# Kernel tuning notes

Hardware: AMD Instinct MI355X
Metric: run time of the kernel (lower is better)

Reference implementation:

```python
import jax, jax.numpy as jnp
import numpy as np

B, C, H, W = 4, 64, 600, 600  # batch, out channels, spatial (H, W divisible by 5)

def setup_inputs() -> dict:
    key = jax.random.key(0)
    k1, k2, k3 = jax.random.split(key, 3)
    x = jax.random.normal(k1, (B, 1, H, W), dtype=jnp.float32)
    # Conv2d(1, channels, kernel_size=3) params; the torch module always uses conv_list[0]
    fan_in = 1 * 3 * 3
    bound = 1.0 / np.sqrt(fan_in)
    weight = jax.random.uniform(k2, (C, 1, 3, 3), dtype=jnp.float32, minval=-bound, maxval=bound)
    bias = jax.random.uniform(k3, (C,), dtype=jnp.float32, minval=-bound, maxval=bound)
    return {"x": x, "weight": weight, "bias": bias}

def reference(x, weight, bias):
    # The 25-phase roll + unfold(stride=5) + fold(stride=3) + conv(stride=3) + strided
    # scatter is exactly a circularly-padded 3x3 stride-1 cross-correlation:
    #   out[b,c,y,xx] = sum_{r,s} weight[c,0,r,s] * x[b,0,(y-1+r)%H,(xx-1+s)%W] + bias[c]
    xp = jnp.pad(x, ((0, 0), (0, 0), (1, 1), (1, 1)), mode="wrap")  # circular pad by 1
    out = jax.lax.conv_general_dilated(
        xp, weight,
        window_strides=(1, 1), padding="VALID",
        dimension_numbers=("NCHW", "OIHW", "NCHW"),
    )
    return out + bias[None, :, None, None]
```

## Files before the change

### kernel.cpp

```cpp
#include <hip/hip_runtime.h>


typedef float v4f __attribute__((ext_vector_type(4)));

#define Bn 4
#define Cn 64
#define Hn 600
#define Wn 600
#define Gn (Wn / 4)
#define TOTAL (Bn * Hn * Gn)

__global__ __launch_bounds__(256) void conv3x3_circ_kernel(
    const float* __restrict__ x,
    const float* __restrict__ w,
    const float* __restrict__ bias,
    float* __restrict__ out)
{
    __shared__ float lw[Cn * 12];
    const int tid = threadIdx.x;
    for (int idx = tid; idx < Cn * 12; idx += 256) {
        const int c = idx / 12;
        const int k = idx - c * 12;
        float v = 0.0f;
        if (k < 9)       v = w[c * 9 + k];
        else if (k == 9) v = bias[c];
        lw[idx] = v;
    }
    __syncthreads();

    const int i = blockIdx.x * 256 + tid;
    if (i >= TOTAL) return;

    const int g  = i % Gn;
    const int t  = i / Gn;
    const int y  = t % Hn;
    const int b  = t / Hn;
    const int x0 = g * 4;

    const int ym = (y == 0)        ? (Hn - 1) : (y - 1);
    const int yp = (y == Hn - 1)   ? 0        : (y + 1);
    const int xm = (x0 == 0)       ? (Wn - 1) : (x0 - 1);
    const int xp = (x0 + 4 == Wn)  ? 0        : (x0 + 4);

    const float* xb = x + (size_t)b * (Hn * Wn);
    const float* rm = xb + ym * Wn;
    const float* rc = xb + y  * Wn;
    const float* rp = xb + yp * Wn;

    float r0[6], r1[6], r2[6];
    v4f m;
    r0[0] = rm[xm]; m = *(const v4f*)(rm + x0);
    r0[1] = m.x; r0[2] = m.y; r0[3] = m.z; r0[4] = m.w; r0[5] = rm[xp];
    r1[0] = rc[xm]; m = *(const v4f*)(rc + x0);
    r1[1] = m.x; r1[2] = m.y; r1[3] = m.z; r1[4] = m.w; r1[5] = rc[xp];
    r2[0] = rp[xm]; m = *(const v4f*)(rp + x0);
    r2[1] = m.x; r2[2] = m.y; r2[3] = m.z; r2[4] = m.w; r2[5] = rp[xp];

    float* op = out + (size_t)b * (Cn * Hn * Wn) + (size_t)y * Wn + x0;
    const v4f* lw4 = (const v4f*)lw;

    #pragma unroll 4
    for (int c = 0; c < Cn; ++c) {
        const v4f wA = lw4[c * 3 + 0];
        const v4f wB = lw4[c * 3 + 1];
        const v4f wC = lw4[c * 3 + 2];
        v4f o;
        #pragma unroll
        for (int j = 0; j < 4; ++j) {
            float a = wC.y;
            a += wA.x * r0[j] + wA.y * r0[j + 1] + wA.z * r0[j + 2];
            a += wA.w * r1[j] + wB.x * r1[j + 1] + wB.y * r1[j + 2];
            a += wB.z * r2[j] + wB.w * r2[j + 1] + wC.x * r2[j + 2];
            o[j] = a;
        }
        __builtin_nontemporal_store(o, (v4f*)op);
        op += Hn * Wn;
    }
}

extern "C" void kernel_launch(void* const* d_in, const int* in_sizes, int n_in,
                              void* d_out, int out_size, void* d_ws, size_t ws_size,
                              hipStream_t stream) {
    const float* x    = (const float*)d_in[0];
    const float* w    = (const float*)d_in[1];
    const float* bias = (const float*)d_in[2];
    float* out        = (float*)d_out;

    const int blocks = (TOTAL + 255) / 256;
    conv3x3_circ_kernel<<<blocks, 256, 0, stream>>>(x, w, bias, out);
}
```

Measured before the change: 370.3 us.

## Parallelize over output channels with one thread per channel-quad and XCD swizzle

```diff
diff --git a/kernel.cpp b/kernel.cpp
--- a/kernel.cpp
+++ b/kernel.cpp
@@ -8,7 +8,10 @@
 #define Hn 600
 #define Wn 600
 #define Gn (Wn / 4)
-#define TOTAL (Bn * Hn * Gn)
+#define QPP (Hn * Gn)
+#define NQ (Bn * Cn * QPP)
+#define NBLK (NQ / 256)
+#define CPX (NBLK / 8)
 
 __global__ __launch_bounds__(256) void conv3x3_circ_kernel(
     const float* __restrict__ x,
@@ -28,19 +31,22 @@
     }
     __syncthreads();
 
-    const int i = blockIdx.x * 256 + tid;
-    if (i >= TOTAL) return;
+    const int bid = blockIdx.x;
+    const int swz = (bid & 7) * CPX + (bid >> 3);
 
-    const int g  = i % Gn;
-    const int t  = i / Gn;
-    const int y  = t % Hn;
-    const int b  = t / Hn;
+    const int q  = swz * 256 + tid;
+    const int p  = q / QPP;
+    const int r  = q - p * QPP;
+    const int y  = r / Gn;
+    const int g  = r - y * Gn;
+    const int c  = p & (Cn - 1);
+    const int b  = p >> 6;
     const int x0 = g * 4;
 
-    const int ym = (y == 0)        ? (Hn - 1) : (y - 1);
-    const int yp = (y == Hn - 1)   ? 0        : (y + 1);
-    const int xm = (x0 == 0)       ? (Wn - 1) : (x0 - 1);
-    const int xp = (x0 + 4 == Wn)  ? 0        : (x0 + 4);
+    const int ym = (y == 0)       ? (Hn - 1) : (y - 1);
+    const int yp = (y == Hn - 1)  ? 0        : (y + 1);
+    const int xm = (x0 == 0)      ? (Wn - 1) : (x0 - 1);
+    const int xp = (x0 + 4 == Wn) ? 0        : (x0 + 4);
 
     const float* xb = x + (size_t)b * (Hn * Wn);
     const float* rm = xb + ym * Wn;
@@ -56,26 +62,22 @@
     r2[0] = rp[xm]; m = *(const v4f*)(rp + x0);
     r2[1] = m.x; r2[2] = m.y; r2[3] = m.z; r2[4] = m.w; r2[5] = rp[xp];
 
-    float* op = out + (size_t)b * (Cn * Hn * Wn) + (size_t)y * Wn + x0;
     const v4f* lw4 = (const v4f*)lw;
+    const v4f wA = lw4[c * 3 + 0];
+    const v4f wB = lw4[c * 3 + 1];
+    const v4f wC = lw4[c * 3 + 2];
 
-    #pragma unroll 4
-    for (int c = 0; c < Cn; ++c) {
-        const v4f wA = lw4[c * 3 + 0];
-        const v4f wB = lw4[c * 3 + 1];
-        const v4f wC = lw4[c * 3 + 2];
-        v4f o;
-        #pragma unroll
-        for (int j = 0; j < 4; ++j) {
-            float a = wC.y;
-            a += wA.x * r0[j] + wA.y * r0[j + 1] + wA.z * r0[j + 2];
-            a += wA.w * r1[j] + wB.x * r1[j + 1] + wB.y * r1[j + 2];
-            a += wB.z * r2[j] + wB.w * r2[j + 1] + wC.x * r2[j + 2];
-            o[j] = a;
-        }
-        __builtin_nontemporal_store(o, (v4f*)op);
-        op += Hn * Wn;
+    v4f o;
+    #pragma unroll
+    for (int j = 0; j < 4; ++j) {
+        float a = wC.y;
+        a += wA.x * r0[j] + wA.y * r0[j + 1] + wA.z * r0[j + 2];
+        a += wA.w * r1[j] + wB.x * r1[j + 1] + wB.y * r1[j + 2];
+        a += wB.z * r2[j] + wB.w * r2[j + 1] + wC.x * r2[j + 2];
+        o[j] = a;
     }
+
+    __builtin_nontemporal_store(o, (v4f*)(out + (size_t)p * (Hn * Wn) + (size_t)y * Wn + x0));
 }
 
 extern "C" void kernel_launch(void* const* d_in, const int* in_sizes, int n_in,
@@ -86,6 +88,5 @@
     const float* bias = (const float*)d_in[2];
     float* out        = (float*)d_out;
 
-    const int blocks = (TOTAL + 255) / 256;
-    conv3x3_circ_kernel<<<blocks, 256, 0, stream>>>(x, w, bias, out);
+    conv3x3_circ_kernel<<<NBLK, 256, 0, stream>>>(x, w, bias, out);
 }
```

Measured after the change: 504.9 us. 1.36x slower.
